# Optimization experiments

Hardware: AMD Instinct MI355X
Metric: run time of the kernel (lower is better)

The kernel has to match this reference:

```python
import jax, jax.numpy as jnp
import numpy as np

B, R, A, K, O, I = 50000, 5, 8, 2, 32, 32


def setup_inputs() -> dict:
    key = jax.random.key(0)
    k1, k2, k3 = jax.random.split(key, 3)
    signal = jax.random.normal(k1, (B, R, A, 3, I), dtype=jnp.float32)
    bary = jax.random.uniform(k2, (B, R, A, 3), dtype=jnp.float32)
    # glorot-uniform-ish kernel: shape (R, A, K, O, I)
    limit = np.sqrt(6.0 / (I + O)).astype(np.float32)
    kernel = jax.random.uniform(k3, (R, A, K, O, I), dtype=jnp.float32,
                                minval=-limit, maxval=limit)
    return {"signal": signal, "bary": bary, "kernel": kernel}


def reference(signal, bary, kernel):
    # Barycentric interpolation: pullback[b,r,a,i] = sum_t bary[b,r,a,t] * signal[b,r,a,t,i]
    pullback = jnp.einsum('brat,brati->brai', bary, signal)  # (B,R,A,I)

    n_rot = kernel.shape[1]  # A rotations
    # rotated angular indices: rot_idx[c, a] = (a + c) % A
    rot_idx = (jnp.arange(n_rot)[:, None] + jnp.arange(n_rot)[None, :]) % n_rot
    k_rot = kernel[:, rot_idx]  # (R, C=A, A, K, O, I)

    # conv[b,c,o] = sum_{r,a,k,i} kernel[r,(a+c)%A,k,o,i] * pullback[b,r,a,i]
    conv = jnp.einsum('brai,rcakoi->bco', pullback, k_rot)  # (B, C, O)
    act = jax.nn.relu(conv)

    # Angular max pooling: pick rotation with max euclidean norm over O
    norms = jnp.linalg.norm(act, axis=-1)          # (B, C)
    best = jnp.argmax(norms, axis=-1)              # (B,)
    out = jnp.take_along_axis(act, best[:, None, None], axis=1)[:, 0]  # (B, O)
    return out
```

## Files before the change

kernel.cpp:

```cpp
#include <hip/hip_runtime.h>


#define B_TOT 50000
#define NRA 40
#define SLOT_B 12288
#define P_OFF  36864

typedef __attribute__((ext_vector_type(8))) short short8v;
typedef __attribute__((ext_vector_type(4))) float f32x4;
typedef const __attribute__((address_space(1))) unsigned int* gp1_t;
typedef __attribute__((address_space(3))) unsigned int* lp3_t;

__device__ __align__(16) unsigned short W_hi_g[NRA * 256 * 32];
__device__ __align__(16) unsigned short W_lo_g[NRA * 256 * 32];

static __device__ __forceinline__ unsigned short f2bf(float x) {
    unsigned u = __float_as_uint(x);
    u += 0x7FFFu + ((u >> 16) & 1u);
    return (unsigned short)(u >> 16);
}
static __device__ __forceinline__ float bf2f(unsigned short h) {
    return __uint_as_float(((unsigned)h) << 16);
}

__global__ __launch_bounds__(256) void build_w_kernel(const float* __restrict__ kern) {
    int e = blockIdx.x * 256 + threadIdx.x;
    int i = e & 31;
    int n = (e >> 5) & 255;
    int ra = e >> 13;
    int r = ra >> 3, a = ra & 7;
    int c = n >> 5, o = n & 31;
    int a2 = (c + a) & 7;
    const float* p = kern + ((((r * 8 + a2) * 2) * 32 + o) * 32 + i);
    float w = p[0] + p[1024];
    unsigned short hi = f2bf(w);
    unsigned short lo = f2bf(w - bf2f(hi));
    W_hi_g[e] = hi;
    W_lo_g[e] = lo;
}

static __device__ __forceinline__ void pcomp(float by0, float by1, float by2,
                                             const float4& a, const float4& b,
                                             const float4& c, float* d) {
    d[0] = fmaf(by2, c.x, fmaf(by1, b.x, by0 * a.x));
    d[1] = fmaf(by2, c.y, fmaf(by1, b.y, by0 * a.y));
    d[2] = fmaf(by2, c.z, fmaf(by1, b.z, by0 * a.z));
    d[3] = fmaf(by2, c.w, fmaf(by1, b.w, by0 * a.w));
}

__global__ __launch_bounds__(256) void conv_geo_kernel(const float* __restrict__ sig,
                                                       const float* __restrict__ bary,
                                                       float* __restrict__ out) {
    __shared__ __align__(16) char lds_raw[45056];

    const int tid  = threadIdx.x;
    const int lane = tid & 63;
    const int wave = tid >> 6;
    const int b_l  = tid >> 2;
    const int q    = tid & 3;
    const int b0   = blockIdx.x * 64;
    int bld = b0 + b_l; if (bld > B_TOT - 1) bld = B_TOT - 1;

    f32x4 acc[4][4];
#pragma unroll
    for (int mi = 0; mi < 4; ++mi)
#pragma unroll
        for (int ni = 0; ni < 4; ++ni) acc[mi][ni] = (f32x4){0.f, 0.f, 0.f, 0.f};

    const int wcol  = (wave * 64 + (lane & 15)) * 32 + (lane >> 4) * 8;
    const int pbase = (lane & 15) * 32 + (lane >> 4) * 8;
    const int widx  = b_l * 32 + q * 4;

    unsigned offA[3], offB[3];
#pragma unroll
    for (int j = 0; j < 3; ++j) {
        int L   = j * 4096 + tid * 16;
        int rIH = L / 384;
        int col = L - rIH * 384;
        int scol = col ^ ((rIH & 7) << 4);
        int r0 = b0 + rIH;      if (r0 > B_TOT - 1) r0 = B_TOT - 1;
        int r1 = b0 + 32 + rIH; if (r1 > B_TOT - 1) r1 = B_TOT - 1;
        offA[j] = (unsigned)r0 * 15360u + (unsigned)scol;
        offB[j] = (unsigned)r1 * 15360u + (unsigned)scol;
    }
    const char* sigc = (const char*)sig;
    auto issueA = [&](int rra, int slot) {
#pragma unroll
        for (int j = 0; j < 3; ++j) {
            const void* gp = sigc + ((size_t)offA[j] + (size_t)rra * 384u);
            void* lp = lds_raw + slot * SLOT_B + j * 4096 + tid * 16;
            __builtin_amdgcn_global_load_lds((gp1_t)gp, (lp3_t)lp, 16, 0, 0);
        }
    };
    auto issueB = [&](int rra, int slot) {
#pragma unroll
        for (int j = 0; j < 3; ++j) {
            const void* gp = sigc + ((size_t)offB[j] + (size_t)rra * 384u);
            void* lp = lds_raw + slot * SLOT_B + j * 4096 + tid * 16;
            __builtin_amdgcn_global_load_lds((gp1_t)gp, (lp3_t)lp, 16, 0, 0);
        }
    };

    issueA(0, 0);
    issueB(0, 1);
    issueA(1, 2);

    int sA = 0, sB = 1;
    unsigned short* p_w = (unsigned short*)(lds_raw + P_OFF);
    const unsigned short* p_r = (const unsigned short*)(lds_raw + P_OFF);
    const int rIHme = b_l & 31;
    const int hfme  = b_l >> 5;
    const int swzP  = (b_l & 7) << 4;

#pragma unroll 1
    for (int ra = 0; ra < NRA; ++ra) {
        if (ra < NRA - 1) asm volatile("s_waitcnt vmcnt(3) lgkmcnt(0)" ::: "memory");
        else              asm volatile("s_waitcnt vmcnt(0) lgkmcnt(0)" ::: "memory");
        __builtin_amdgcn_s_barrier();
        asm volatile("" ::: "memory");

        const float* bp = bary + (size_t)bld * 120 + ra * 3;
        float by0 = bp[0], by1 = bp[1], by2 = bp[2];
        short8v bh[4], bl[4];
        {
            const unsigned short* wh = W_hi_g + ra * 8192 + wcol;
            const unsigned short* wl = W_lo_g + ra * 8192 + wcol;
#pragma unroll
            for (int ni = 0; ni < 4; ++ni) {
                bh[ni] = *(const short8v*)(wh + ni * 512);
                bl[ni] = *(const short8v*)(wl + ni * 512);
            }
        }

        {
            int slotSel = hfme ? sB : sA;
            const char* rowp = lds_raw + slotSel * SLOT_B + rIHme * 384;
            float4 s0 = *(const float4*)(rowp + ((q * 16)      ^ swzP));
            float4 s1 = *(const float4*)(rowp + ((q * 16 + 64) ^ swzP));
            float4 s2 = *(const float4*)(rowp + (((q * 16)      ^ swzP) + 128));
            float4 s3 = *(const float4*)(rowp + (((q * 16 + 64) ^ swzP) + 128));
            float4 s4 = *(const float4*)(rowp + (((q * 16)      ^ swzP) + 256));
            float4 s5 = *(const float4*)(rowp + (((q * 16 + 64) ^ swzP) + 256));
            float pa[4], pb2[4];
            pcomp(by0, by1, by2, s0, s2, s4, pa);
            pcomp(by0, by1, by2, s1, s3, s5, pb2);
            unsigned short h1[4], l1[4], h2[4], l2[4];
#pragma unroll
            for (int k = 0; k < 4; ++k) {
                h1[k] = f2bf(pa[k]);  l1[k] = f2bf(pa[k]  - bf2f(h1[k]));
                h2[k] = f2bf(pb2[k]); l2[k] = f2bf(pb2[k] - bf2f(h2[k]));
            }
            uint2 H1, H2, L1, L2;
            H1.x = (unsigned)h1[0] | ((unsigned)h1[1] << 16);
            H1.y = (unsigned)h1[2] | ((unsigned)h1[3] << 16);
            H2.x = (unsigned)h2[0] | ((unsigned)h2[1] << 16);
            H2.y = (unsigned)h2[2] | ((unsigned)h2[3] << 16);
            L1.x = (unsigned)l1[0] | ((unsigned)l1[1] << 16);
            L1.y = (unsigned)l1[2] | ((unsigned)l1[3] << 16);
            L2.x = (unsigned)l2[0] | ((unsigned)l2[1] << 16);
            L2.y = (unsigned)l2[2] | ((unsigned)l2[3] << 16);
            *(uint2*)(p_w + widx)               = H1;
            *(uint2*)(p_w + widx + 16)          = H2;
            *(uint2*)(p_w + 2048 + widx)        = L1;
            *(uint2*)(p_w + 2048 + widx + 16)   = L2;
        }

        asm volatile("s_waitcnt lgkmcnt(0)" ::: "memory");
        __builtin_amdgcn_s_barrier();
        asm volatile("" ::: "memory");

        if (ra + 1 < NRA) issueB(ra + 1, sA);
        if (ra + 2 < NRA) issueA(ra + 2, sB);
        sA += 2; if (sA >= 3) sA -= 3;
        sB += 2; if (sB >= 3) sB -= 3;

#pragma unroll
        for (int mi = 0; mi < 4; ++mi) {
            const unsigned short* pr = p_r + mi * 512 + pbase;
            short8v ah = *(const short8v*)pr;
            short8v al = *(const short8v*)(pr + 2048);
#pragma unroll
            for (int ni = 0; ni < 4; ++ni) {
                acc[mi][ni] = __builtin_amdgcn_mfma_f32_16x16x32_bf16(ah, bh[ni], acc[mi][ni], 0, 0, 0);
                acc[mi][ni] = __builtin_amdgcn_mfma_f32_16x16x32_bf16(ah, bl[ni], acc[mi][ni], 0, 0, 0);
                acc[mi][ni] = __builtin_amdgcn_mfma_f32_16x16x32_bf16(al, bh[ni], acc[mi][ni], 0, 0, 0);
            }
        }
    }

    float* smem = (float*)lds_raw;
    const int colb = wave * 64 + (lane & 15);
    const int rsub = (lane >> 4) * 4;
#pragma unroll
    for (int ph = 0; ph < 2; ++ph) {
        __syncthreads();
#pragma unroll
        for (int mh = 0; mh < 2; ++mh) {
            int mi = ph * 2 + mh;
#pragma unroll
            for (int ni = 0; ni < 4; ++ni)
#pragma unroll
                for (int j = 0; j < 4; ++j)
                    smem[(mh * 16 + rsub + j) * 264 + colb + ni * 16] =
                        fmaxf(acc[mi][ni][j], 0.0f);
        }
        __syncthreads();
        int bb = tid >> 3;
        int c  = tid & 7;
        float n2 = 0.0f;
#pragma unroll
        for (int t = 0; t < 8; ++t) {
            float4 v = *(const float4*)&smem[bb * 264 + c * 32 + t * 4];
            n2 = fmaf(v.x, v.x, n2); n2 = fmaf(v.y, v.y, n2);
            n2 = fmaf(v.z, v.z, n2); n2 = fmaf(v.w, v.w, n2);
        }
        int bc = c;
#pragma unroll
        for (int m = 1; m < 8; m <<= 1) {
            float on2 = __shfl_xor(n2, m, 64);
            int obc = __shfl_xor(bc, m, 64);
            if (on2 > n2 || (on2 == n2 && obc < bc)) { n2 = on2; bc = obc; }
        }
        int b = b0 + ph * 32 + bb;
        if (b < B_TOT) {
            float4 v = *(const float4*)&smem[bb * 264 + bc * 32 + (tid & 7) * 4];
            *(float4*)&out[(size_t)b * 32 + (tid & 7) * 4] = v;
        }
    }
}

extern "C" void kernel_launch(void* const* d_in, const int* in_sizes, int n_in,
                              void* d_out, int out_size, void* d_ws, size_t ws_size,
                              hipStream_t stream) {
    const float* sig  = (const float*)d_in[0];
    const float* bary = (const float*)d_in[1];
    const float* kern = (const float*)d_in[2];
    float* out = (float*)d_out;

    build_w_kernel<<<(NRA * 256 * 32) / 256, 256, 0, stream>>>(kern);
    conv_geo_kernel<<<(B_TOT + 63) / 64, 256, 0, stream>>>(sig, bary, out);
}
```

Measured before the change: 229.1 us.

## Halve batch tile to 32 and process two (r,a) slices per pipeline stage

Result: slower. 252.6 us (+10.3%).

```diff
diff --git a/kernel.cpp b/kernel.cpp
--- a/kernel.cpp
+++ b/kernel.cpp
@@ -3,8 +3,9 @@
 
 #define B_TOT 50000
 #define NRA 40
-#define SLOT_B 12288
-#define P_OFF  36864
+#define NSTG 20
+#define SLOT_B 24576
+#define P_OFF  49152
 
 typedef __attribute__((ext_vector_type(8))) short short8v;
 typedef __attribute__((ext_vector_type(4))) float f32x4;
@@ -51,96 +52,82 @@
 __global__ __launch_bounds__(256) void conv_geo_kernel(const float* __restrict__ sig,
                                                        const float* __restrict__ bary,
                                                        float* __restrict__ out) {
-    __shared__ __align__(16) char lds_raw[45056];
+    __shared__ __align__(16) char lds_raw[59392];
 
     const int tid  = threadIdx.x;
     const int lane = tid & 63;
     const int wave = tid >> 6;
-    const int b_l  = tid >> 2;
-    const int q    = tid & 3;
-    const int b0   = blockIdx.x * 64;
-    int bld = b0 + b_l; if (bld > B_TOT - 1) bld = B_TOT - 1;
-
-    f32x4 acc[4][4];
-#pragma unroll
-    for (int mi = 0; mi < 4; ++mi)
+    const int b0   = blockIdx.x * 32;
+
+    f32x4 acc[2][4];
+#pragma unroll
+    for (int mi = 0; mi < 2; ++mi)
 #pragma unroll
         for (int ni = 0; ni < 4; ++ni) acc[mi][ni] = (f32x4){0.f, 0.f, 0.f, 0.f};
 
-    const int wcol  = (wave * 64 + (lane & 15)) * 32 + (lane >> 4) * 8;
-    const int pbase = (lane & 15) * 32 + (lane >> 4) * 8;
-    const int widx  = b_l * 32 + q * 4;
-
-    unsigned offA[3], offB[3];
-#pragma unroll
-    for (int j = 0; j < 3; ++j) {
+    const int wcol = (wave * 64 + (lane & 15)) * 32 + (lane >> 4) * 8;
+    const int poff = (lane & 15) * 40 + (lane >> 4) * 8;
+
+    unsigned soff[6];
+#pragma unroll
+    for (int j = 0; j < 6; ++j) {
         int L   = j * 4096 + tid * 16;
-        int rIH = L / 384;
-        int col = L - rIH * 384;
-        int scol = col ^ ((rIH & 7) << 4);
-        int r0 = b0 + rIH;      if (r0 > B_TOT - 1) r0 = B_TOT - 1;
-        int r1 = b0 + 32 + rIH; if (r1 > B_TOT - 1) r1 = B_TOT - 1;
-        offA[j] = (unsigned)r0 * 15360u + (unsigned)scol;
-        offB[j] = (unsigned)r1 * 15360u + (unsigned)scol;
+        int row = L / 768;
+        int col = L - row * 768;
+        int scol = col ^ ((row & 7) << 4);
+        int b = b0 + row; if (b > B_TOT - 1) b = B_TOT - 1;
+        soff[j] = (unsigned)b * 15360u + (unsigned)scol;
     }
     const char* sigc = (const char*)sig;
-    auto issueA = [&](int rra, int slot) {
-#pragma unroll
-        for (int j = 0; j < 3; ++j) {
-            const void* gp = sigc + ((size_t)offA[j] + (size_t)rra * 384u);
+    auto issue = [&](int g, int slot) {
+#pragma unroll
+        for (int j = 0; j < 6; ++j) {
+            const void* gp = sigc + ((size_t)soff[j] + (size_t)g * 768u);
             void* lp = lds_raw + slot * SLOT_B + j * 4096 + tid * 16;
             __builtin_amdgcn_global_load_lds((gp1_t)gp, (lp3_t)lp, 16, 0, 0);
         }
     };
-    auto issueB = [&](int rra, int slot) {
-#pragma unroll
-        for (int j = 0; j < 3; ++j) {
-            const void* gp = sigc + ((size_t)offB[j] + (size_t)rra * 384u);
-            void* lp = lds_raw + slot * SLOT_B + j * 4096 + tid * 16;
-            __builtin_amdgcn_global_load_lds((gp1_t)gp, (lp3_t)lp, 16, 0, 0);
-        }
-    };
-
-    issueA(0, 0);
-    issueB(0, 1);
-    issueA(1, 2);
-
-    int sA = 0, sB = 1;
-    unsigned short* p_w = (unsigned short*)(lds_raw + P_OFF);
-    const unsigned short* p_r = (const unsigned short*)(lds_raw + P_OFF);
-    const int rIHme = b_l & 31;
-    const int hfme  = b_l >> 5;
-    const int swzP  = (b_l & 7) << 4;
+
+    issue(0, 0);
+    issue(1, 1);
+
+    const int pr_row = tid >> 3;
+    const int pr_s   = (tid >> 2) & 1;
+    const int pr_q   = tid & 3;
+    const int pr_swz = (pr_row & 7) << 4;
+    int pbv = b0 + pr_row; if (pbv > B_TOT - 1) pbv = B_TOT - 1;
+    unsigned short* p_h = (unsigned short*)(lds_raw + P_OFF);
 
 #pragma unroll 1
-    for (int ra = 0; ra < NRA; ++ra) {
-        if (ra < NRA - 1) asm volatile("s_waitcnt vmcnt(3) lgkmcnt(0)" ::: "memory");
+    for (int g = 0; g < NSTG; ++g) {
+        const int slot = g & 1;
+        if (g < NSTG - 1) asm volatile("s_waitcnt vmcnt(6) lgkmcnt(0)" ::: "memory");
         else              asm volatile("s_waitcnt vmcnt(0) lgkmcnt(0)" ::: "memory");
         __builtin_amdgcn_s_barrier();
         asm volatile("" ::: "memory");
 
-        const float* bp = bary + (size_t)bld * 120 + ra * 3;
+        short8v bh[2][4], bl[2][4];
+#pragma unroll
+        for (int s = 0; s < 2; ++s) {
+            const unsigned short* wh = W_hi_g + (2 * g + s) * 8192 + wcol;
+            const unsigned short* wl = W_lo_g + (2 * g + s) * 8192 + wcol;
+#pragma unroll
+            for (int ni = 0; ni < 4; ++ni) {
+                bh[s][ni] = *(const short8v*)(wh + ni * 512);
+                bl[s][ni] = *(const short8v*)(wl + ni * 512);
+            }
+        }
+        const float* bp = bary + (size_t)pbv * 120 + (2 * g + pr_s) * 3;
         float by0 = bp[0], by1 = bp[1], by2 = bp[2];
-        short8v bh[4], bl[4];
+
         {
-            const unsigned short* wh = W_hi_g + ra * 8192 + wcol;
-            const unsigned short* wl = W_lo_g + ra * 8192 + wcol;
-#pragma unroll
-            for (int ni = 0; ni < 4; ++ni) {
-                bh[ni] = *(const short8v*)(wh + ni * 512);
-                bl[ni] = *(const short8v*)(wl + ni * 512);
-            }
-        }
-
-        {
-            int slotSel = hfme ? sB : sA;
-            const char* rowp = lds_raw + slotSel * SLOT_B + rIHme * 384;
-            float4 s0 = *(const float4*)(rowp + ((q * 16)      ^ swzP));
-            float4 s1 = *(const float4*)(rowp + ((q * 16 + 64) ^ swzP));
-            float4 s2 = *(const float4*)(rowp + (((q * 16)      ^ swzP) + 128));
-            float4 s3 = *(const float4*)(rowp + (((q * 16 + 64) ^ swzP) + 128));
-            float4 s4 = *(const float4*)(rowp + (((q * 16)      ^ swzP) + 256));
-            float4 s5 = *(const float4*)(rowp + (((q * 16 + 64) ^ swzP) + 256));
+            const char* rowp = lds_raw + slot * SLOT_B + pr_row * 768 + pr_s * 384;
+            float4 s0 = *(const float4*)(rowp + ((pr_q * 16)      ^ pr_swz));
+            float4 s1 = *(const float4*)(rowp + ((pr_q * 16 + 64) ^ pr_swz));
+            float4 s2 = *(const float4*)(rowp + 128 + ((pr_q * 16)      ^ pr_swz));
+            float4 s3 = *(const float4*)(rowp + 128 + ((pr_q * 16 + 64) ^ pr_swz));
+            float4 s4 = *(const float4*)(rowp + 256 + ((pr_q * 16)      ^ pr_swz));
+            float4 s5 = *(const float4*)(rowp + 256 + ((pr_q * 16 + 64) ^ pr_swz));
             float pa[4], pb2[4];
             pcomp(by0, by1, by2, s0, s2, s4, pa);
             pcomp(by0, by1, by2, s1, s3, s5, pb2);
@@ -159,52 +146,49 @@
             L1.y = (unsigned)l1[2] | ((unsigned)l1[3] << 16);
             L2.x = (unsigned)l2[0] | ((unsigned)l2[1] << 16);
             L2.y = (unsigned)l2[2] | ((unsigned)l2[3] << 16);
-            *(uint2*)(p_w + widx)               = H1;
-            *(uint2*)(p_w + widx + 16)          = H2;
-            *(uint2*)(p_w + 2048 + widx)        = L1;
-            *(uint2*)(p_w + 2048 + widx + 16)   = L2;
+            int widx = pr_s * 1280 + pr_row * 40 + pr_q * 4;
+            *(uint2*)(p_h + widx)             = H1;
+            *(uint2*)(p_h + widx + 16)        = H2;
+            *(uint2*)(p_h + 2560 + widx)      = L1;
+            *(uint2*)(p_h + 2560 + widx + 16) = L2;
         }
 
         asm volatile("s_waitcnt lgkmcnt(0)" ::: "memory");
         __builtin_amdgcn_s_barrier();
         asm volatile("" ::: "memory");
 
-        if (ra + 1 < NRA) issueB(ra + 1, sA);
-        if (ra + 2 < NRA) issueA(ra + 2, sB);
-        sA += 2; if (sA >= 3) sA -= 3;
-        sB += 2; if (sB >= 3) sB -= 3;
-
-#pragma unroll
-        for (int mi = 0; mi < 4; ++mi) {
-            const unsigned short* pr = p_r + mi * 512 + pbase;
-            short8v ah = *(const short8v*)pr;
-            short8v al = *(const short8v*)(pr + 2048);
-#pragma unroll
-            for (int ni = 0; ni < 4; ++ni) {
-                acc[mi][ni] = __builtin_amdgcn_mfma_f32_16x16x32_bf16(ah, bh[ni], acc[mi][ni], 0, 0, 0);
-                acc[mi][ni] = __builtin_amdgcn_mfma_f32_16x16x32_bf16(ah, bl[ni], acc[mi][ni], 0, 0, 0);
-                acc[mi][ni] = __builtin_amdgcn_mfma_f32_16x16x32_bf16(al, bh[ni], acc[mi][ni], 0, 0, 0);
+        if (g + 2 < NSTG) issue(g + 2, slot);
+
+#pragma unroll
+        for (int s = 0; s < 2; ++s)
+#pragma unroll
+            for (int mi = 0; mi < 2; ++mi) {
+                const unsigned short* pr_ = p_h + s * 1280 + mi * 640 + poff;
+                short8v ah = *(const short8v*)pr_;
+                short8v al = *(const short8v*)(pr_ + 2560);
+#pragma unroll
+                for (int ni = 0; ni < 4; ++ni) {
+                    acc[mi][ni] = __builtin_amdgcn_mfma_f32_16x16x32_bf16(ah, bh[s][ni], acc[mi][ni], 0, 0, 0);
+                    acc[mi][ni] = __builtin_amdgcn_mfma_f32_16x16x32_bf16(ah, bl[s][ni], acc[mi][ni], 0, 0, 0);
+                    acc[mi][ni] = __builtin_amdgcn_mfma_f32_16x16x32_bf16(al, bh[s][ni], acc[mi][ni], 0, 0, 0);
+                }
             }
-        }
     }
 
     float* smem = (float*)lds_raw;
     const int colb = wave * 64 + (lane & 15);
     const int rsub = (lane >> 4) * 4;
-#pragma unroll
-    for (int ph = 0; ph < 2; ++ph) {
-        __syncthreads();
-#pragma unroll
-        for (int mh = 0; mh < 2; ++mh) {
-            int mi = ph * 2 + mh;
-#pragma unroll
-            for (int ni = 0; ni < 4; ++ni)
-#pragma unroll
-                for (int j = 0; j < 4; ++j)
-                    smem[(mh * 16 + rsub + j) * 264 + colb + ni * 16] =
-                        fmaxf(acc[mi][ni][j], 0.0f);
-        }
-        __syncthreads();
+    __syncthreads();
+#pragma unroll
+    for (int mi = 0; mi < 2; ++mi)
+#pragma unroll
+        for (int ni = 0; ni < 4; ++ni)
+#pragma unroll
+            for (int j = 0; j < 4; ++j)
+                smem[(mi * 16 + rsub + j) * 264 + colb + ni * 16] =
+                    fmaxf(acc[mi][ni][j], 0.0f);
+    __syncthreads();
+    {
         int bb = tid >> 3;
         int c  = tid & 7;
         float n2 = 0.0f;
@@ -221,7 +205,7 @@
             int obc = __shfl_xor(bc, m, 64);
             if (on2 > n2 || (on2 == n2 && obc < bc)) { n2 = on2; bc = obc; }
         }
-        int b = b0 + ph * 32 + bb;
+        int b = b0 + bb;
         if (b < B_TOT) {
             float4 v = *(const float4*)&smem[bb * 264 + bc * 32 + (tid & 7) * 4];
             *(float4*)&out[(size_t)b * 32 + (tid & 7) * 4] = v;
@@ -238,5 +222,5 @@
     float* out = (float*)d_out;
 
     build_w_kernel<<<(NRA * 256 * 32) / 256, 256, 0, stream>>>(kern);
-    conv_geo_kernel<<<(B_TOT + 63) / 64, 256, 0, stream>>>(sig, bary, out);
-}
+    conv_geo_kernel<<<(B_TOT + 31) / 32, 256, 0, stream>>>(sig, bary, out);
+}
```
